# Performance work log

Measured on AMD Instinct MI355X. Metric: run time of the kernel, lower is better.

The kernel has to match this reference:

```python
import jax, jax.numpy as jnp
import numpy as np

LRELU_SLOPE = 0.2
EPS = 1e-6

def _conv1x1(x, w):
    # x: [B,C,N,K], w: [O,C] -> [B,O,N,K]
    return jnp.einsum('bcnk,oc->bonk', x, w)

def _affine(x, g, b):
    # eval-mode BatchNorm with running mean=0, var=1 -> pure affine
    return x * g[None, :, None, None] + b[None, :, None, None]

def _lrelu(x):
    return jnp.where(x >= 0, x, LRELU_SLOPE * x)

def _head(x, w1, g, b, w2, b2):
    # Conv2d(2C,8,1,no bias) -> BN -> LeakyReLU -> (Dropout=id) -> Conv2d(8,1,1,bias)
    h = _lrelu(_affine(_conv1x1(x, w1), g, b))
    return _conv1x1(h, w2) + b2[None, :, None, None]  # [B,1,N,K]

def setup_inputs() -> dict:
    key = jax.random.key(0)
    ks = jax.random.split(key, 16)
    B, C2, N, K, O, H = 8, 128, 4096, 32, 64, 8
    inp = {
        'x': jax.random.normal(ks[0], (B, C2, N, K), jnp.float32),
        'w_trans': jax.random.normal(ks[1], (O, C2), jnp.float32) * 0.05,
        'g_trans': jax.random.uniform(ks[2], (O,), jnp.float32) + 0.5,
        'b_trans': jax.random.normal(ks[3], (O,), jnp.float32) * 0.1,
        'w_gate1': jax.random.normal(ks[4], (H, C2), jnp.float32) * 0.05,
        'g_gate': jax.random.uniform(ks[5], (H,), jnp.float32) + 0.5,
        'b_gate': jax.random.normal(ks[6], (H,), jnp.float32) * 0.1,
        'w_gate2': jax.random.normal(ks[7], (1, H), jnp.float32) * 0.3,
        'b_gate2': jax.random.normal(ks[8], (1,), jnp.float32) * 0.1,
        'w_attn1': jax.random.normal(ks[9], (H, C2), jnp.float32) * 0.05,
        'g_attn': jax.random.uniform(ks[10], (H,), jnp.float32) + 0.5,
        'b_attn': jax.random.normal(ks[11], (H,), jnp.float32) * 0.1,
        'w_attn2': jax.random.normal(ks[12], (1, H), jnp.float32) * 0.3,
        'b_attn2': jax.random.normal(ks[13], (1,), jnp.float32) * 0.1,
        'agg_alpha': jnp.zeros((), jnp.float32),
    }
    return inp

def reference(x, w_trans, g_trans, b_trans, w_gate1, g_gate, b_gate, w_gate2, b_gate2,
              w_attn1, g_attn, b_attn, w_attn2, b_attn2, agg_alpha):
    # mode='full', eval mode, tau=1.0, hard=False
    trans_feat = _lrelu(_affine(_conv1x1(x, w_trans), g_trans, b_trans))  # [B,O,N,K]
    gate_logits = _head(x, w_gate1, g_gate, b_gate, w_gate2, b_gate2)     # [B,1,N,K]
    # eval-mode gumbel_sigmoid_sample -> deterministic binary mask
    mask = (gate_logits >= 0).astype(x.dtype)                             # [B,1,N,K]
    attn_logits = _head(x, w_attn1, g_attn, b_attn, w_attn2, b_attn2)     # [B,1,N,K]
    attn_logits = attn_logits - jnp.max(attn_logits, axis=-1, keepdims=True)
    weights = jax.nn.softmax(attn_logits, axis=-1)
    # soft (hard=False) path: mask then renormalize
    weights = weights * mask
    weights = weights / (jnp.sum(weights, axis=-1, keepdims=True) + EPS)
    out_sum = jnp.sum(trans_feat * weights, axis=-1)   # [B,O,N]
    out_max = jnp.max(trans_feat, axis=-1)             # [B,O,N] (no masking when hard=False)
    alpha = jax.nn.sigmoid(agg_alpha)
    out = alpha * out_sum + (1.0 - alpha) * out_max
    return out, gate_logits
```

## Files before the change

### kernel.cpp

```cpp
#include <hip/hip_runtime.h>
#include <math.h>

#define NPB 131072
#define NOUT 80
#define LRELU_SLOPE 0.2f
#define EPSV 1e-6f

__global__ __launch_bounds__(256) void wt_kernel(
    const float* __restrict__ w_trans,
    const float* __restrict__ w_gate1,
    const float* __restrict__ w_attn1,
    float* __restrict__ WT)
{
    int i = blockIdx.x * 256 + threadIdx.x;
    if (i >= 128 * NOUT) return;
    int c = i / NOUT;
    int o = i - c * NOUT;
    float v;
    if (o < 64)      v = w_trans[o * 128 + c];
    else if (o < 72) v = w_gate1[(o - 64) * 128 + c];
    else             v = w_attn1[(o - 72) * 128 + c];
    WT[i] = v;
}

__global__ __launch_bounds__(256, 4) void gsl_kernel(
    const float* __restrict__ x,
    const float* __restrict__ WT,
    const float* __restrict__ g_trans, const float* __restrict__ b_trans,
    const float* __restrict__ g_gate,  const float* __restrict__ b_gate,
    const float* __restrict__ w_gate2, const float* __restrict__ b_gate2,
    const float* __restrict__ g_attn,  const float* __restrict__ b_attn,
    const float* __restrict__ w_attn2, const float* __restrict__ b_attn2,
    const float* __restrict__ agg_alpha,
    float* __restrict__ out0,
    float* __restrict__ outg)
{
    const int tid = threadIdx.x;
    const size_t p = (size_t)blockIdx.x * 256 + tid;
    const int b   = (int)(p >> 17);
    const int pin = (int)(p & (NPB - 1));
    const int n   = pin >> 5;

    const float* xp = x + (size_t)b * 128 * NPB + pin;

    float acc[NOUT];
#pragma unroll
    for (int o = 0; o < NOUT; ++o) acc[o] = 0.f;

#pragma unroll 1
    for (int c0 = 0; c0 < 128; c0 += 8) {
        float xv[8];
#pragma unroll
        for (int i = 0; i < 8; ++i)
            xv[i] = xp[(size_t)(c0 + i) * NPB];
#pragma unroll
        for (int i = 0; i < 8; ++i) {
            const float* wc = WT + (size_t)(c0 + i) * NOUT;
#pragma unroll
            for (int o = 0; o < NOUT; ++o)
                acc[o] = fmaf(wc[o], xv[i], acc[o]);
        }
    }

    float gl = b_gate2[0];
#pragma unroll
    for (int h = 0; h < 8; ++h) {
        float v = fmaf(acc[64 + h], g_gate[h], b_gate[h]);
        v = (v >= 0.f) ? v : LRELU_SLOPE * v;
        gl = fmaf(w_gate2[h], v, gl);
    }
    float al = b_attn2[0];
#pragma unroll
    for (int h = 0; h < 8; ++h) {
        float v = fmaf(acc[72 + h], g_attn[h], b_attn[h]);
        v = (v >= 0.f) ? v : LRELU_SLOPE * v;
        al = fmaf(w_attn2[h], v, al);
    }
    outg[p] = gl;

#pragma unroll
    for (int o = 0; o < 64; ++o) {
        float v = fmaf(acc[o], g_trans[o], b_trans[o]);
        acc[o] = (v >= 0.f) ? v : LRELU_SLOPE * v;
    }

    float m = al;
#pragma unroll
    for (int s = 1; s < 32; s <<= 1) m = fmaxf(m, __shfl_xor(m, s, 32));
    float e = expf(al - m);
    float s1 = e;
#pragma unroll
    for (int s = 1; s < 32; s <<= 1) s1 += __shfl_xor(s1, s, 32);
    float w0 = e / s1;
    float wm = (gl >= 0.f) ? w0 : 0.f;
    float s2 = wm;
#pragma unroll
    for (int s = 1; s < 32; s <<= 1) s2 += __shfl_xor(s2, s, 32);
    const float wgt = wm / (s2 + EPSV);

    const float alpha = 1.f / (1.f + expf(-agg_alpha[0]));
    const float beta  = 1.f - alpha;

    const int lk = tid & 31;
    float* outp = out0 + ((size_t)b * 64) * 4096 + n;

#pragma unroll
    for (int o = 0; o < 64; ++o) {
        float sv = acc[o] * wgt;
        float mv = acc[o];
#pragma unroll
        for (int s = 1; s < 32; s <<= 1) {
            sv += __shfl_xor(sv, s, 32);
            mv = fmaxf(mv, __shfl_xor(mv, s, 32));
        }
        if (lk == (o & 31))
            outp[(size_t)o * 4096] = fmaf(alpha, sv, beta * mv);
    }
}

extern "C" void kernel_launch(void* const* d_in, const int* in_sizes, int n_in,
                              void* d_out, int out_size, void* d_ws, size_t ws_size,
                              hipStream_t stream) {
    const float* x        = (const float*)d_in[0];
    const float* w_trans  = (const float*)d_in[1];
    const float* g_trans  = (const float*)d_in[2];
    const float* b_trans  = (const float*)d_in[3];
    const float* w_gate1  = (const float*)d_in[4];
    const float* g_gate   = (const float*)d_in[5];
    const float* b_gate   = (const float*)d_in[6];
    const float* w_gate2  = (const float*)d_in[7];
    const float* b_gate2  = (const float*)d_in[8];
    const float* w_attn1  = (const float*)d_in[9];
    const float* g_attn   = (const float*)d_in[10];
    const float* b_attn   = (const float*)d_in[11];
    const float* w_attn2  = (const float*)d_in[12];
    const float* b_attn2  = (const float*)d_in[13];
    const float* agg_alpha= (const float*)d_in[14];

    float* out0 = (float*)d_out;
    float* outg = (float*)d_out + (size_t)8*64*4096;
    float* WT   = (float*)d_ws;

    wt_kernel<<<(128*NOUT + 255)/256, 256, 0, stream>>>(w_trans, w_gate1, w_attn1, WT);

    const int npix = 8 * NPB;
    gsl_kernel<<<npix/256, 256, 0, stream>>>(
        x, WT, g_trans, b_trans, g_gate, b_gate, w_gate2, b_gate2,
        g_attn, b_attn, w_attn2, b_attn2, agg_alpha, out0, outg);
}
```

Baseline: 860.0 us.

## Compute the 1x1 convolutions with split-bf16 MFMA instead of scalar FMAs

The fused 128→80 channel projection now runs on the matrix cores. It uses 16x16x32 bf16 MFMA with a three-term hi/lo split (hi*hi + lo*hi + hi*lo) to keep close to fp32 accuracy. Each wave handles one 32-neighbor pixel group and prefetches x with a register double buffer. The softmax and aggregation reductions are restructured to use 16-lane shuffles on the MFMA output layout. This is meant to remove the large scalar FMA cost of the original per-thread 80-output loop, at the price of bf16 split error, three MFMAs per product and lower occupancy (launch bounds 3).

```diff
diff --git a/kernel.cpp b/kernel.cpp
--- a/kernel.cpp
+++ b/kernel.cpp
@@ -2,30 +2,43 @@
 #include <math.h>
 
 #define NPB 131072
-#define NOUT 80
 #define LRELU_SLOPE 0.2f
 #define EPSV 1e-6f
+
+typedef __attribute__((ext_vector_type(8))) short short8;
+typedef __attribute__((ext_vector_type(4))) float f32x4;
+
+static __device__ __forceinline__ unsigned short f2bf_rne(float f) {
+    unsigned int u = __float_as_uint(f);
+    u += 0x7fffu + ((u >> 16) & 1u);
+    return (unsigned short)(u >> 16);
+}
 
 __global__ __launch_bounds__(256) void wt_kernel(
     const float* __restrict__ w_trans,
     const float* __restrict__ w_gate1,
     const float* __restrict__ w_attn1,
-    float* __restrict__ WT)
+    unsigned short* __restrict__ Whi,
+    unsigned short* __restrict__ Wlo)
 {
     int i = blockIdx.x * 256 + threadIdx.x;
-    if (i >= 128 * NOUT) return;
-    int c = i / NOUT;
-    int o = i - c * NOUT;
+    if (i >= 80 * 128) return;
+    int o = i >> 7;
+    int c = i & 127;
     float v;
     if (o < 64)      v = w_trans[o * 128 + c];
     else if (o < 72) v = w_gate1[(o - 64) * 128 + c];
     else             v = w_attn1[(o - 72) * 128 + c];
-    WT[i] = v;
-}
-
-__global__ __launch_bounds__(256, 4) void gsl_kernel(
+    unsigned int u = __float_as_uint(v);
+    Whi[i] = (unsigned short)(u >> 16);
+    float hif = __uint_as_float(u & 0xffff0000u);
+    Wlo[i] = f2bf_rne(v - hif);
+}
+
+__global__ __launch_bounds__(256, 3) void gsl_kernel(
     const float* __restrict__ x,
-    const float* __restrict__ WT,
+    const unsigned short* __restrict__ Whi,
+    const unsigned short* __restrict__ Wlo,
     const float* __restrict__ g_trans, const float* __restrict__ b_trans,
     const float* __restrict__ g_gate,  const float* __restrict__ b_gate,
     const float* __restrict__ w_gate2, const float* __restrict__ b_gate2,
@@ -35,86 +48,168 @@
     float* __restrict__ out0,
     float* __restrict__ outg)
 {
-    const int tid = threadIdx.x;
-    const size_t p = (size_t)blockIdx.x * 256 + tid;
-    const int b   = (int)(p >> 17);
-    const int pin = (int)(p & (NPB - 1));
+    const int tid  = threadIdx.x;
+    const int wid  = tid >> 6;
+    const int lane = tid & 63;
+    const int g    = lane >> 4;
+    const int col  = lane & 15;
+
+    const size_t p0 = (size_t)blockIdx.x * 128 + (size_t)wid * 32;
+    const int b   = (int)(p0 >> 17);
+    const int pin = (int)(p0 & (NPB - 1));
     const int n   = pin >> 5;
 
-    const float* xp = x + (size_t)b * 128 * NPB + pin;
-
-    float acc[NOUT];
-#pragma unroll
-    for (int o = 0; o < NOUT; ++o) acc[o] = 0.f;
+    const float* xq = x + (size_t)b * 128 * NPB + pin + col;
+
+    f32x4 acc[5][2];
+#pragma unroll
+    for (int ot = 0; ot < 5; ++ot) {
+        acc[ot][0] = (f32x4){0.f, 0.f, 0.f, 0.f};
+        acc[ot][1] = (f32x4){0.f, 0.f, 0.f, 0.f};
+    }
+
+    float cur[16];
+    {
+        const int cb = 8 * g;
+#pragma unroll
+        for (int j = 0; j < 8; ++j) cur[j]     = xq[(size_t)(cb + j) * NPB];
+#pragma unroll
+        for (int j = 0; j < 8; ++j) cur[8 + j] = xq[(size_t)(cb + j) * NPB + 16];
+    }
 
 #pragma unroll 1
-    for (int c0 = 0; c0 < 128; c0 += 8) {
-        float xv[8];
-#pragma unroll
-        for (int i = 0; i < 8; ++i)
-            xv[i] = xp[(size_t)(c0 + i) * NPB];
-#pragma unroll
-        for (int i = 0; i < 8; ++i) {
-            const float* wc = WT + (size_t)(c0 + i) * NOUT;
-#pragma unroll
-            for (int o = 0; o < NOUT; ++o)
-                acc[o] = fmaf(wc[o], xv[i], acc[o]);
-        }
-    }
-
-    float gl = b_gate2[0];
-#pragma unroll
-    for (int h = 0; h < 8; ++h) {
-        float v = fmaf(acc[64 + h], g_gate[h], b_gate[h]);
-        v = (v >= 0.f) ? v : LRELU_SLOPE * v;
-        gl = fmaf(w_gate2[h], v, gl);
-    }
-    float al = b_attn2[0];
-#pragma unroll
-    for (int h = 0; h < 8; ++h) {
-        float v = fmaf(acc[72 + h], g_attn[h], b_attn[h]);
-        v = (v >= 0.f) ? v : LRELU_SLOPE * v;
-        al = fmaf(w_attn2[h], v, al);
-    }
-    outg[p] = gl;
-
-#pragma unroll
-    for (int o = 0; o < 64; ++o) {
-        float v = fmaf(acc[o], g_trans[o], b_trans[o]);
-        acc[o] = (v >= 0.f) ? v : LRELU_SLOPE * v;
-    }
-
-    float m = al;
-#pragma unroll
-    for (int s = 1; s < 32; s <<= 1) m = fmaxf(m, __shfl_xor(m, s, 32));
-    float e = expf(al - m);
-    float s1 = e;
-#pragma unroll
-    for (int s = 1; s < 32; s <<= 1) s1 += __shfl_xor(s1, s, 32);
-    float w0 = e / s1;
-    float wm = (gl >= 0.f) ? w0 : 0.f;
-    float s2 = wm;
-#pragma unroll
-    for (int s = 1; s < 32; s <<= 1) s2 += __shfl_xor(s2, s, 32);
-    const float wgt = wm / (s2 + EPSV);
-
-    const float alpha = 1.f / (1.f + expf(-agg_alpha[0]));
+    for (int kk = 0; kk < 4; ++kk) {
+        const int cbase = kk * 32 + 8 * g;
+
+        float nxt[16];
+        if (kk < 3) {
+            const int cb2 = cbase + 32;
+#pragma unroll
+            for (int j = 0; j < 8; ++j) nxt[j]     = xq[(size_t)(cb2 + j) * NPB];
+#pragma unroll
+            for (int j = 0; j < 8; ++j) nxt[8 + j] = xq[(size_t)(cb2 + j) * NPB + 16];
+        }
+
+        short8 ahi[5], alo5[5];
+#pragma unroll
+        for (int ot = 0; ot < 5; ++ot) {
+            const int wof = (ot * 16 + col) * 128 + cbase;
+            ahi[ot]  = *(const short8*)(Whi + wof);
+            alo5[ot] = *(const short8*)(Wlo + wof);
+        }
+
+        union U { unsigned int u[4]; short8 s; };
+        U bh0, bl0, bh1, bl1;
+#pragma unroll
+        for (int jj = 0; jj < 4; ++jj) {
+            float a0 = cur[2 * jj], a1 = cur[2 * jj + 1];
+            unsigned int ua0 = __float_as_uint(a0), ua1 = __float_as_uint(a1);
+            bh0.u[jj] = (ua1 & 0xffff0000u) | (ua0 >> 16);
+            float r0 = a0 - __uint_as_float(ua0 & 0xffff0000u);
+            float r1 = a1 - __uint_as_float(ua1 & 0xffff0000u);
+            bl0.u[jj] = ((unsigned int)f2bf_rne(r1) << 16) | (unsigned int)f2bf_rne(r0);
+
+            float c0v = cur[8 + 2 * jj], c1v = cur[8 + 2 * jj + 1];
+            unsigned int uc0 = __float_as_uint(c0v), uc1 = __float_as_uint(c1v);
+            bh1.u[jj] = (uc1 & 0xffff0000u) | (uc0 >> 16);
+            float s0 = c0v - __uint_as_float(uc0 & 0xffff0000u);
+            float s1v = c1v - __uint_as_float(uc1 & 0xffff0000u);
+            bl1.u[jj] = ((unsigned int)f2bf_rne(s1v) << 16) | (unsigned int)f2bf_rne(s0);
+        }
+
+#pragma unroll
+        for (int ot = 0; ot < 5; ++ot) {
+            acc[ot][0] = __builtin_amdgcn_mfma_f32_16x16x32_bf16(ahi[ot],  bh0.s, acc[ot][0], 0, 0, 0);
+            acc[ot][1] = __builtin_amdgcn_mfma_f32_16x16x32_bf16(ahi[ot],  bh1.s, acc[ot][1], 0, 0, 0);
+            acc[ot][0] = __builtin_amdgcn_mfma_f32_16x16x32_bf16(alo5[ot], bh0.s, acc[ot][0], 0, 0, 0);
+            acc[ot][1] = __builtin_amdgcn_mfma_f32_16x16x32_bf16(alo5[ot], bh1.s, acc[ot][1], 0, 0, 0);
+            acc[ot][0] = __builtin_amdgcn_mfma_f32_16x16x32_bf16(ahi[ot],  bl0.s, acc[ot][0], 0, 0, 0);
+            acc[ot][1] = __builtin_amdgcn_mfma_f32_16x16x32_bf16(ahi[ot],  bl1.s, acc[ot][1], 0, 0, 0);
+        }
+
+        if (kk < 3) {
+#pragma unroll
+            for (int j = 0; j < 16; ++j) cur[j] = nxt[j];
+        }
+    }
+
+    const bool isGate = (g < 2);
+    const int hbase = (g & 1) * 4;
+    float hg[4], hb[4], hw[4];
+#pragma unroll
+    for (int r = 0; r < 4; ++r) {
+        const int h = hbase + r;
+        hg[r] = isGate ? g_gate[h]  : g_attn[h];
+        hb[r] = isGate ? b_gate[h]  : b_attn[h];
+        hw[r] = isGate ? w_gate2[h] : w_attn2[h];
+    }
+    float part0 = 0.f, part1 = 0.f;
+#pragma unroll
+    for (int r = 0; r < 4; ++r) {
+        float v0 = fmaf(acc[4][0][r], hg[r], hb[r]);
+        v0 = (v0 >= 0.f) ? v0 : LRELU_SLOPE * v0;
+        part0 = fmaf(hw[r], v0, part0);
+        float v1 = fmaf(acc[4][1][r], hg[r], hb[r]);
+        v1 = (v1 >= 0.f) ? v1 : LRELU_SLOPE * v1;
+        part1 = fmaf(hw[r], v1, part1);
+    }
+    float t0 = part0 + __shfl_xor(part0, 16);
+    float t1 = part1 + __shfl_xor(part1, 16);
+    float q0 = __shfl_xor(t0, 32);
+    float q1 = __shfl_xor(t1, 32);
+    const float bg2 = b_gate2[0], ba2 = b_attn2[0];
+    float gl0 = (isGate ? t0 : q0) + bg2;
+    float gl1 = (isGate ? t1 : q1) + bg2;
+    float al0 = (isGate ? q0 : t0) + ba2;
+    float al1 = (isGate ? q1 : t1) + ba2;
+
+    if (lane < 16) {
+        outg[p0 + col]      = gl0;
+        outg[p0 + 16 + col] = gl1;
+    }
+
+    float m = fmaxf(al0, al1);
+#pragma unroll
+    for (int s = 1; s < 16; s <<= 1) m = fmaxf(m, __shfl_xor(m, s));
+    float e0 = expf(al0 - m), e1 = expf(al1 - m);
+    float w0m = (gl0 >= 0.f) ? e0 : 0.f;
+    float w1m = (gl1 >= 0.f) ? e1 : 0.f;
+    float s1 = e0 + e1;
+    float sm = w0m + w1m;
+#pragma unroll
+    for (int s = 1; s < 16; s <<= 1) {
+        s1 += __shfl_xor(s1, s);
+        sm += __shfl_xor(sm, s);
+    }
+    const float inv = 1.f / (sm + EPSV * s1);
+    const float wgt0 = w0m * inv;
+    const float wgt1 = w1m * inv;
+
+    const float aa = agg_alpha[0];
+    const float alpha = 1.f / (1.f + expf(-aa));
     const float beta  = 1.f - alpha;
 
-    const int lk = tid & 31;
-    float* outp = out0 + ((size_t)b * 64) * 4096 + n;
-
-#pragma unroll
-    for (int o = 0; o < 64; ++o) {
-        float sv = acc[o] * wgt;
-        float mv = acc[o];
-#pragma unroll
-        for (int s = 1; s < 32; s <<= 1) {
-            sv += __shfl_xor(sv, s, 32);
-            mv = fmaxf(mv, __shfl_xor(mv, s, 32));
-        }
-        if (lk == (o & 31))
-            outp[(size_t)o * 4096] = fmaf(alpha, sv, beta * mv);
+    float* outb = out0 + (size_t)b * 64 * 4096 + n;
+#pragma unroll
+    for (int ot = 0; ot < 4; ++ot) {
+#pragma unroll
+        for (int r = 0; r < 4; ++r) {
+            const int o = ot * 16 + 4 * g + r;
+            const float gt = g_trans[o], bt = b_trans[o];
+            float v0 = fmaf(acc[ot][0][r], gt, bt);
+            v0 = (v0 >= 0.f) ? v0 : LRELU_SLOPE * v0;
+            float v1 = fmaf(acc[ot][1][r], gt, bt);
+            v1 = (v1 >= 0.f) ? v1 : LRELU_SLOPE * v1;
+            float sv = fmaf(v0, wgt0, v1 * wgt1);
+            float mv = fmaxf(v0, v1);
+#pragma unroll
+            for (int s = 1; s < 16; s <<= 1) {
+                sv += __shfl_xor(sv, s);
+                mv = fmaxf(mv, __shfl_xor(mv, s));
+            }
+            if (col == 0)
+                outb[(size_t)o * 4096] = fmaf(alpha, sv, beta * mv);
+        }
     }
 }
 
@@ -139,12 +234,13 @@
 
     float* out0 = (float*)d_out;
     float* outg = (float*)d_out + (size_t)8*64*4096;
-    float* WT   = (float*)d_ws;
-
-    wt_kernel<<<(128*NOUT + 255)/256, 256, 0, stream>>>(w_trans, w_gate1, w_attn1, WT);
+    unsigned short* Whi = (unsigned short*)d_ws;
+    unsigned short* Wlo = Whi + 80 * 128;
+
+    wt_kernel<<<(80*128 + 255)/256, 256, 0, stream>>>(w_trans, w_gate1, w_attn1, Whi, Wlo);
 
     const int npix = 8 * NPB;
-    gsl_kernel<<<npix/256, 256, 0, stream>>>(
-        x, WT, g_trans, b_trans, g_gate, b_gate, w_gate2, b_gate2,
+    gsl_kernel<<<npix / 128, 256, 0, stream>>>(
+        x, Whi, Wlo, g_trans, b_trans, g_gate, b_gate, w_gate2, b_gate2,
         g_attn, b_attn, w_attn2, b_attn2, agg_alpha, out0, outg);
 }
```

After: 837.0 us. 1.03x faster.
